# Optimization experiments

Hardware: AMD Instinct MI355X
Metric: run time of the kernel (lower is better)

Reference implementation:

```python
import jax, jax.numpy as jnp
import numpy as np
import math

B, LQ, LK = 2, 2048, 2048
DIM = 1024
H = 16
DH = DIM // H


def setup_inputs() -> dict:
    key = jax.random.key(0)
    ks = jax.random.split(key, 12)
    s = 1.0 / math.sqrt(DIM)
    return {
        "query": jax.random.normal(ks[0], (B, LQ, DIM), jnp.float32),
        "key": jax.random.normal(ks[1], (B, LK, DIM), jnp.float32),
        "value": jax.random.normal(ks[2], (B, LK, DIM), jnp.float32),
        "mask": jnp.zeros((B, LQ, LK), dtype=bool),
        "Wq": jax.random.normal(ks[3], (DIM, DIM), jnp.float32) * s,
        "bq": jax.random.normal(ks[4], (DIM,), jnp.float32) * s,
        "Wk": jax.random.normal(ks[5], (DIM, DIM), jnp.float32) * s,
        "bk": jax.random.normal(ks[6], (DIM,), jnp.float32) * s,
        "Wv": jax.random.normal(ks[7], (DIM, DIM), jnp.float32) * s,
        "bv": jax.random.normal(ks[8], (DIM,), jnp.float32) * s,
        "Wo": jax.random.normal(ks[9], (DIM, DIM), jnp.float32) * s,
        "bo": jax.random.normal(ks[10], (DIM,), jnp.float32) * s,
    }


def reference(query, key, value, mask, Wq, bq, Wk, bk, Wv, bv, Wo, bo):
    b = query.shape[0]

    def shape(x):  # (b, l, dim) -> (b, h, l, dh)
        return x.reshape(b, -1, H, DH).transpose(0, 2, 1, 3)

    q = shape(query @ Wq.T + bq)
    k = shape(key @ Wk.T + bk)
    v = shape(value @ Wv.T + bv)

    q = q / math.sqrt(DH)
    # (b, h, lq, lk) score matrix, computed in float32 as the original does
    scores = jnp.einsum("bhqd,bhkd->bhqk", q, k).astype(jnp.float32)
    scores = jnp.where(mask[:, None, :, :], jnp.float32(-1e18), scores)
    attn = jax.nn.softmax(scores, axis=-1).astype(q.dtype)
    context = jnp.einsum("bhqk,bhkd->bhqd", attn, v)
    context = context.transpose(0, 2, 1, 3).reshape(b, -1, H * DH)
    return context @ Wo.T + bo
```

## Files before the change

kernel.cpp:

```cpp
#include <hip/hip_runtime.h>
#include <hip/hip_bf16.h>

typedef __attribute__((ext_vector_type(4))) float float4v;
typedef __attribute__((ext_vector_type(8))) __bf16 bf16x8;
typedef __attribute__((ext_vector_type(4))) unsigned short ushort4v;

#define MFMA16(a, b, c) __builtin_amdgcn_mfma_f32_16x16x32_bf16(a, b, c, 0, 0, 0)

__device__ __forceinline__ unsigned short f2bf(float f) {
    return __builtin_bit_cast(unsigned short, (__bf16)f);
}

__device__ __forceinline__ float fast_exp2(float x) {
#if __has_builtin(__builtin_amdgcn_exp2f)
    return __builtin_amdgcn_exp2f(x);
#else
    return exp2f(x);
#endif
}

__device__ __forceinline__ void gl_lds16(const unsigned short* g, unsigned short* l) {
    __builtin_amdgcn_global_load_lds(
        (const __attribute__((address_space(1))) void*)g,
        (__attribute__((address_space(3))) void*)l, 16, 0, 0);
}

__device__ __forceinline__ uint4 pack8bf(float4v a0, float4v a1) {
    uint4 u;
    u.x = (unsigned int)f2bf(a0.x) | ((unsigned int)f2bf(a0.y) << 16);
    u.y = (unsigned int)f2bf(a0.z) | ((unsigned int)f2bf(a0.w) << 16);
    u.z = (unsigned int)f2bf(a1.x) | ((unsigned int)f2bf(a1.y) << 16);
    u.w = (unsigned int)f2bf(a1.z) | ((unsigned int)f2bf(a1.w) << 16);
    return u;
}

struct CvtSeg { const float* s; unsigned short* d; int n; };
struct Cvt4 { CvtSeg seg[4]; };

__global__ __launch_bounds__(256) void cvt_kernel(Cvt4 a) {
    const CvtSeg c = a.seg[blockIdx.y];
    const int stride = gridDim.x * 256 * 4;
    for (int i = (blockIdx.x * 256 + threadIdx.x) * 4; i < c.n; i += stride) {
        float4v v = *(const float4v*)(c.s + i);
        ushort4v u;
        u.x = f2bf(v.x); u.y = f2bf(v.y); u.z = f2bf(v.z); u.w = f2bf(v.w);
        *(ushort4v*)(c.d + i) = u;
    }
}

__global__ __launch_bounds__(256) void gemm_qkv_kernel(
    const float* qa, const float* ka, const float* va,
    const unsigned short* Wqb, const unsigned short* Wkb, const unsigned short* Wvb,
    const float* bq, const float* bk, const float* bv,
    unsigned short* Qb, unsigned short* Kb, unsigned short* Vtg, float qscale) {
    __shared__ unsigned short Sm[17408];
    unsigned short* As = Sm;
    unsigned short* Ws = Sm + 8192;

    const int z = blockIdx.z;
    const float* A = z == 0 ? qa : (z == 1 ? ka : va);
    const unsigned short* W = z == 0 ? Wqb : (z == 1 ? Wkb : Wvb);
    const float* bias = z == 0 ? bq : (z == 1 ? bk : bv);
    const float scale = z == 0 ? qscale : 1.0f;

    const int K = 1024, N = 1024;
    const int t = threadIdx.x;
    const int w = t >> 6, lane = t & 63;
    const int quad = lane >> 4, l16 = lane & 15;
    const int m0 = blockIdx.x * 128, n0 = blockIdx.y * 128;
    const int wm = (w >> 1) * 64, wn = (w & 1) * 64;

    float4v acc[4][4];
    for (int i = 0; i < 4; ++i)
        for (int j = 0; j < 4; ++j) acc[i][j] = float4v{0.f, 0.f, 0.f, 0.f};

    const int arow = t >> 3, acol = (t & 7) * 8;
    const int srow = lane >> 3, scol = (lane & 7) * 8;

    for (int k0 = 0; k0 < K; k0 += 64) {
        __syncthreads();
        for (int p = 0; p < 4; ++p) {
            const int r = arow + p * 32;
            const float* ap = A + (size_t)(m0 + r) * K + k0 + acol;
            float4v a0 = *(const float4v*)ap;
            float4v a1 = *(const float4v*)(ap + 4);
            *(uint4*)&As[r * 64 + acol] = pack8bf(a0, a1);
        }
        for (int i = 0; i < 4; ++i) {
            const int c = w * 4 + i;
            gl_lds16(W + (size_t)(n0 + c * 8 + srow) * K + k0 + scol,
                     &Ws[c * 512 + lane * 8]);
        }
        __syncthreads();
        for (int ks = 0; ks < 2; ++ks) {
            bf16x8 af[4], wf[4];
            for (int i = 0; i < 4; ++i)
                af[i] = *(const bf16x8*)&As[(wm + i * 16 + l16) * 64 + ks * 32 + quad * 8];
            for (int i = 0; i < 4; ++i)
                wf[i] = *(const bf16x8*)&Ws[(wn + i * 16 + l16) * 64 + ks * 32 + quad * 8];
            for (int mi = 0; mi < 4; ++mi)
                for (int ni = 0; ni < 4; ++ni)
                    acc[mi][ni] = MFMA16(af[mi], wf[ni], acc[mi][ni]);
        }
    }

    if (z < 2) {
        unsigned short* C = z == 0 ? Qb : Kb;
        for (int mi = 0; mi < 4; ++mi)
            for (int ni = 0; ni < 4; ++ni) {
                const int col = n0 + wn + ni * 16 + l16;
                const float bvv = bias[col];
                for (int reg = 0; reg < 4; ++reg) {
                    const int row = m0 + wm + mi * 16 + quad * 4 + reg;
                    C[(size_t)row * N + col] = f2bf((acc[mi][ni][reg] + bvv) * scale);
                }
            }
    } else {
        __syncthreads();
        for (int mi = 0; mi < 4; ++mi)
            for (int ni = 0; ni < 4; ++ni) {
                const int col = wn + ni * 16 + l16;
                const float bvv = bias[n0 + col];
                for (int reg = 0; reg < 4; ++reg) {
                    const int row = wm + mi * 16 + quad * 4 + reg;
                    Sm[col * 136 + row] = f2bf(acc[mi][ni][reg] + bvv);
                }
            }
        __syncthreads();
        const int col = t >> 1, rb = (t & 1) * 64;
        for (int j = 0; j < 8; ++j) {
            uint4 v = *(const uint4*)&Sm[col * 136 + rb + j * 8];
            *(uint4*)&Vtg[(size_t)(n0 + col) * 4096 + m0 + rb + j * 8] = v;
        }
    }
}

__global__ __launch_bounds__(256) void gemm_out_kernel(const unsigned short* __restrict__ A,
                                                       const unsigned short* __restrict__ W,
                                                       const float* __restrict__ bias,
                                                       float* __restrict__ Cout) {
    __shared__ unsigned short As[64 * 64];
    __shared__ unsigned short Ws[128 * 64];
    const int N = 1024, K = 1024;
    const int t = threadIdx.x;
    const int w = t >> 6, lane = t & 63;
    const int quad = lane >> 4, l16 = lane & 15;
    const int m0 = blockIdx.x * 64, n0 = blockIdx.y * 128;
    const int wm = (w & 1) * 32, wn = (w >> 1) * 64;

    float4v acc[2][4];
    for (int i = 0; i < 2; ++i)
        for (int j = 0; j < 4; ++j) acc[i][j] = float4v{0.f, 0.f, 0.f, 0.f};

    const int srow = lane >> 3;
    const int scol = (lane & 7) * 8;

    for (int k0 = 0; k0 < K; k0 += 64) {
        __syncthreads();
        for (int i = 0; i < 2; ++i) {
            const int c = w * 2 + i;
            gl_lds16(A + (size_t)(m0 + c * 8 + srow) * K + k0 + scol,
                     &As[c * 512 + lane * 8]);
        }
        for (int i = 0; i < 4; ++i) {
            const int c = w * 4 + i;
            gl_lds16(W + (size_t)(n0 + c * 8 + srow) * K + k0 + scol,
                     &Ws[c * 512 + lane * 8]);
        }
        __syncthreads();
        for (int ks = 0; ks < 2; ++ks) {
            bf16x8 af[2], wf[4];
            for (int i = 0; i < 2; ++i)
                af[i] = *(const bf16x8*)&As[(wm + i * 16 + l16) * 64 + ks * 32 + quad * 8];
            for (int i = 0; i < 4; ++i)
                wf[i] = *(const bf16x8*)&Ws[(wn + i * 16 + l16) * 64 + ks * 32 + quad * 8];
            for (int mi = 0; mi < 2; ++mi)
                for (int ni = 0; ni < 4; ++ni)
                    acc[mi][ni] = MFMA16(af[mi], wf[ni], acc[mi][ni]);
        }
    }

    for (int mi = 0; mi < 2; ++mi)
        for (int ni = 0; ni < 4; ++ni) {
            const int col = n0 + wn + ni * 16 + l16;
            const float bv = bias[col];
            for (int reg = 0; reg < 4; ++reg) {
                const int row = m0 + wm + mi * 16 + quad * 4 + reg;
                Cout[(size_t)row * N + col] = acc[mi][ni][reg] + bv;
            }
        }
}

__global__ __launch_bounds__(256) void attn_kernel(const unsigned short* __restrict__ Q,
                                                   const unsigned short* __restrict__ Kg,
                                                   const unsigned short* __restrict__ Vtg,
                                                   const unsigned char* __restrict__ mask,
                                                   unsigned short* __restrict__ Ctx) {
    const int bid = blockIdx.x;
    const int bh = bid & 31;
    const int qt = bid >> 5;
    const int b = bh >> 4, h = bh & 15;
    const int t = threadIdx.x, w = t >> 6, lane = t & 63;
    const int quad = lane >> 4, l16 = lane & 15;

    __shared__ unsigned short Pt[128][72];
    __shared__ unsigned short Ks[64][72];
    __shared__ unsigned short Vt[64][72];

    const unsigned short* Qp = Q + ((size_t)(b * 2048 + qt * 128)) * 1024 + h * 64;
    const unsigned short* Kp = Kg + ((size_t)b * 2048) * 1024 + h * 64;
    const unsigned short* Vp = Vtg + (size_t)(h * 64) * 4096 + b * 2048;
    const unsigned char* Mp = mask + (size_t)(b * 2048 + qt * 128) * 2048;

    for (int p = 0; p < 4; ++p) {
        const int idx = t + p * 256;
        const int r = idx >> 3, c8 = (idx & 7) * 8;
        *(uint4*)&Pt[r][c8] = *(const uint4*)(Qp + (size_t)r * 1024 + c8);
    }
    __syncthreads();
    bf16x8 qf[2][2];
    for (int c = 0; c < 2; ++c)
        for (int ks = 0; ks < 2; ++ks)
            qf[c][ks] = *(const bf16x8*)&Pt[w * 32 + c * 16 + l16][ks * 32 + quad * 8];

    float4v o[2][4];
    for (int c = 0; c < 2; ++c)
        for (int i = 0; i < 4; ++i) o[c][i] = float4v{0.f, 0.f, 0.f, 0.f};
    float l_acc[2] = {0.f, 0.f};

    const int sr = t >> 3, sc8 = (t & 7) * 8;
    const int vd = t >> 2, vs0 = (t & 3) * 16;
    const int mrow = w * 32 + (lane >> 1);
    const int mc0 = (lane & 1) * 32;

    uint4 kreg0, kreg1, vreg0, vreg1, mreg0, mreg1;
    {
        kreg0 = *(const uint4*)(Kp + (size_t)sr * 1024 + sc8);
        kreg1 = *(const uint4*)(Kp + (size_t)(sr + 32) * 1024 + sc8);
        vreg0 = *(const uint4*)(Vp + (size_t)vd * 4096 + vs0);
        vreg1 = *(const uint4*)(Vp + (size_t)vd * 4096 + vs0 + 8);
        mreg0 = *(const uint4*)(Mp + (size_t)mrow * 2048 + mc0);
        mreg1 = *(const uint4*)(Mp + (size_t)mrow * 2048 + mc0 + 16);
    }

    for (int kc = 0; kc < 2048; kc += 64) {
        __syncthreads();
        *(uint4*)&Ks[sr][sc8] = kreg0;
        *(uint4*)&Ks[sr + 32][sc8] = kreg1;
        *(uint4*)&Vt[vd][vs0] = vreg0;
        *(uint4*)&Vt[vd][vs0 + 8] = vreg1;
        const unsigned int mor = mreg0.x | mreg0.y | mreg0.z | mreg0.w |
                                 mreg1.x | mreg1.y | mreg1.z | mreg1.w;
        const bool anymask = __any(mor != 0);
        __syncthreads();

        const int kn = kc + 64;
        if (kn < 2048) {
            kreg0 = *(const uint4*)(Kp + (size_t)(kn + sr) * 1024 + sc8);
            kreg1 = *(const uint4*)(Kp + (size_t)(kn + sr + 32) * 1024 + sc8);
            vreg0 = *(const uint4*)(Vp + (size_t)vd * 4096 + kn + vs0);
            vreg1 = *(const uint4*)(Vp + (size_t)vd * 4096 + kn + vs0 + 8);
            mreg0 = *(const uint4*)(Mp + (size_t)mrow * 2048 + kn + mc0);
            mreg1 = *(const uint4*)(Mp + (size_t)mrow * 2048 + kn + mc0 + 16);
        }

        float4v s0[4], s1[4];
        for (int nt = 0; nt < 4; ++nt) {
            const float4v z4 = float4v{0.f, 0.f, 0.f, 0.f};
            bf16x8 kf = *(const bf16x8*)&Ks[nt * 16 + l16][quad * 8];
            s0[nt] = MFMA16(kf, qf[0][0], z4);
            s1[nt] = MFMA16(kf, qf[1][0], z4);
            kf = *(const bf16x8*)&Ks[nt * 16 + l16][32 + quad * 8];
            s0[nt] = MFMA16(kf, qf[0][1], s0[nt]);
            s1[nt] = MFMA16(kf, qf[1][1], s1[nt]);
        }

        for (int c = 0; c < 2; ++c) {
            float4v* s = c ? s1 : s0;
            const int qrow = w * 32 + c * 16 + l16;
            float lc = l_acc[c];
            for (int nt = 0; nt < 4; ++nt) {
                float p0 = s[nt][0], p1 = s[nt][1], p2 = s[nt][2], p3 = s[nt][3];
                if (anymask) {
                    const unsigned char* mr =
                        Mp + (size_t)qrow * 2048 + kc + nt * 16 + quad * 4;
                    if (mr[0]) p0 = -1e18f;
                    if (mr[1]) p1 = -1e18f;
                    if (mr[2]) p2 = -1e18f;
                    if (mr[3]) p3 = -1e18f;
                }
                const float e0 = fast_exp2(p0), e1 = fast_exp2(p1);
                const float e2 = fast_exp2(p2), e3 = fast_exp2(p3);
                lc += (e0 + e1) + (e2 + e3);
                uint2 u;
                u.x = (unsigned int)f2bf(e0) | ((unsigned int)f2bf(e1) << 16);
                u.y = (unsigned int)f2bf(e2) | ((unsigned int)f2bf(e3) << 16);
                *(uint2*)&Pt[qrow][nt * 16 + quad * 4] = u;
            }
            l_acc[c] = lc;
        }

        for (int ks = 0; ks < 2; ++ks) {
            bf16x8 pf0 = *(const bf16x8*)&Pt[w * 32 + l16][ks * 32 + quad * 8];
            bf16x8 pf1 = *(const bf16x8*)&Pt[w * 32 + 16 + l16][ks * 32 + quad * 8];
            for (int dt = 0; dt < 4; ++dt) {
                bf16x8 vf = *(const bf16x8*)&Vt[dt * 16 + l16][ks * 32 + quad * 8];
                o[0][dt] = MFMA16(pf0, vf, o[0][dt]);
                o[1][dt] = MFMA16(pf1, vf, o[1][dt]);
            }
        }
    }

    float lfull[2];
    for (int c = 0; c < 2; ++c) {
        float l = l_acc[c];
        l += __shfl_xor(l, 16);
        l += __shfl_xor(l, 32);
        lfull[c] = l;
    }

    for (int c = 0; c < 2; ++c) {
        float inv[4];
        for (int reg = 0; reg < 4; ++reg)
            inv[reg] = 1.0f / __shfl(lfull[c], (lane & 48) | (quad * 4 + reg));
        for (int dt = 0; dt < 4; ++dt) {
            const int dcol = dt * 16 + l16;
            for (int reg = 0; reg < 4; ++reg) {
                const int ql = w * 32 + c * 16 + quad * 4 + reg;
                Ctx[((size_t)(b * 2048 + qt * 128 + ql)) * 1024 + h * 64 + dcol] =
                    f2bf(o[c][dt][reg] * inv[reg]);
            }
        }
    }
}

extern "C" void kernel_launch(void* const* d_in, const int* in_sizes, int n_in,
                              void* d_out, int out_size, void* d_ws, size_t ws_size,
                              hipStream_t stream) {
    (void)in_sizes; (void)n_in; (void)out_size; (void)ws_size;
    const float* query = (const float*)d_in[0];
    const float* key   = (const float*)d_in[1];
    const float* value = (const float*)d_in[2];
    const unsigned char* mask = (const unsigned char*)d_in[3];
    const float* Wq = (const float*)d_in[4];
    const float* bq = (const float*)d_in[5];
    const float* Wk = (const float*)d_in[6];
    const float* bk = (const float*)d_in[7];
    const float* Wv = (const float*)d_in[8];
    const float* bv = (const float*)d_in[9];
    const float* Wo = (const float*)d_in[10];
    const float* bo = (const float*)d_in[11];

    const size_t MD = (size_t)4096 * 1024;
    const size_t WD = (size_t)1024 * 1024;

    unsigned short* Qb  = (unsigned short*)d_ws;
    unsigned short* Kb  = Qb + MD;
    unsigned short* Vtg = Kb + MD;
    unsigned short* Wqb = Vtg + MD;
    unsigned short* Wkb = Wqb + WD;
    unsigned short* Wvb = Wkb + WD;
    unsigned short* Wob = Wvb + WD;
    unsigned short* Cb  = Wob + WD;

    Cvt4 cv;
    cv.seg[0] = {Wq, Wqb, (int)WD};
    cv.seg[1] = {Wk, Wkb, (int)WD};
    cv.seg[2] = {Wv, Wvb, (int)WD};
    cv.seg[3] = {Wo, Wob, (int)WD};
    cvt_kernel<<<dim3(256, 4), 256, 0, stream>>>(cv);

    const float qscale = 0.125f * 1.44269504088896f;
    gemm_qkv_kernel<<<dim3(32, 8, 3), 256, 0, stream>>>(
        query, key, value, Wqb, Wkb, Wvb, bq, bk, bv, Qb, Kb, Vtg, qscale);

    attn_kernel<<<dim3(512), 256, 0, stream>>>(Qb, Kb, Vtg, mask, Cb);

    gemm_out_kernel<<<dim3(64, 8), 256, 0, stream>>>(Cb, Wob, bo, (float*)d_out);
}
```

Measured before the change: 287.0 us.

## Register-prefetch next K tile in projection GEMMs instead of direct global-to-LDS loads

Both the QKV projection GEMM and the output projection GEMM stop using global_load_lds for each K tile. They now load the next tile's A and W slices into registers while the MFMA loop runs on the current tile, then write them to LDS at the start of the next iteration. This is meant to hide global memory latency behind compute. The cost is extra registers for the prefetch buffers, which may lower occupancy, and extra LDS store instructions.

```diff
diff --git a/kernel.cpp b/kernel.cpp
--- a/kernel.cpp
+++ b/kernel.cpp
@@ -17,12 +17,6 @@
 #else
     return exp2f(x);
 #endif
-}
-
-__device__ __forceinline__ void gl_lds16(const unsigned short* g, unsigned short* l) {
-    __builtin_amdgcn_global_load_lds(
-        (const __attribute__((address_space(1))) void*)g,
-        (__attribute__((address_space(3))) void*)l, 16, 0, 0);
 }
 
 __device__ __forceinline__ uint4 pack8bf(float4v a0, float4v a1) {
@@ -77,21 +71,41 @@
     const int arow = t >> 3, acol = (t & 7) * 8;
     const int srow = lane >> 3, scol = (lane & 7) * 8;
 
-    for (int k0 = 0; k0 < K; k0 += 64) {
-        __syncthreads();
+    float4v apre[4][2];
+    uint4 wpre[4];
+    {
         for (int p = 0; p < 4; ++p) {
-            const int r = arow + p * 32;
-            const float* ap = A + (size_t)(m0 + r) * K + k0 + acol;
-            float4v a0 = *(const float4v*)ap;
-            float4v a1 = *(const float4v*)(ap + 4);
-            *(uint4*)&As[r * 64 + acol] = pack8bf(a0, a1);
+            const float* ap = A + (size_t)(m0 + arow + p * 32) * K + acol;
+            apre[p][0] = *(const float4v*)ap;
+            apre[p][1] = *(const float4v*)(ap + 4);
         }
         for (int i = 0; i < 4; ++i) {
             const int c = w * 4 + i;
-            gl_lds16(W + (size_t)(n0 + c * 8 + srow) * K + k0 + scol,
-                     &Ws[c * 512 + lane * 8]);
-        }
-        __syncthreads();
+            wpre[i] = *(const uint4*)(W + (size_t)(n0 + c * 8 + srow) * K + scol);
+        }
+    }
+
+    for (int k0 = 0; k0 < K; k0 += 64) {
+        __syncthreads();
+        for (int p = 0; p < 4; ++p)
+            *(uint4*)&As[(arow + p * 32) * 64 + acol] = pack8bf(apre[p][0], apre[p][1]);
+        for (int i = 0; i < 4; ++i)
+            *(uint4*)&Ws[(w * 4 + i) * 512 + lane * 8] = wpre[i];
+        __syncthreads();
+
+        const int kn = k0 + 64;
+        if (kn < K) {
+            for (int p = 0; p < 4; ++p) {
+                const float* ap = A + (size_t)(m0 + arow + p * 32) * K + kn + acol;
+                apre[p][0] = *(const float4v*)ap;
+                apre[p][1] = *(const float4v*)(ap + 4);
+            }
+            for (int i = 0; i < 4; ++i) {
+                const int c = w * 4 + i;
+                wpre[i] = *(const uint4*)(W + (size_t)(n0 + c * 8 + srow) * K + kn + scol);
+            }
+        }
+
         for (int ks = 0; ks < 2; ++ks) {
             bf16x8 af[4], wf[4];
             for (int i = 0; i < 4; ++i)
@@ -155,19 +169,38 @@
     const int srow = lane >> 3;
     const int scol = (lane & 7) * 8;
 
-    for (int k0 = 0; k0 < K; k0 += 64) {
-        __syncthreads();
+    uint4 apre[2], wpre[4];
+    {
         for (int i = 0; i < 2; ++i) {
             const int c = w * 2 + i;
-            gl_lds16(A + (size_t)(m0 + c * 8 + srow) * K + k0 + scol,
-                     &As[c * 512 + lane * 8]);
+            apre[i] = *(const uint4*)(A + (size_t)(m0 + c * 8 + srow) * K + scol);
         }
         for (int i = 0; i < 4; ++i) {
             const int c = w * 4 + i;
-            gl_lds16(W + (size_t)(n0 + c * 8 + srow) * K + k0 + scol,
-                     &Ws[c * 512 + lane * 8]);
-        }
-        __syncthreads();
+            wpre[i] = *(const uint4*)(W + (size_t)(n0 + c * 8 + srow) * K + scol);
+        }
+    }
+
+    for (int k0 = 0; k0 < K; k0 += 64) {
+        __syncthreads();
+        for (int i = 0; i < 2; ++i)
+            *(uint4*)&As[(w * 2 + i) * 512 + lane * 8] = apre[i];
+        for (int i = 0; i < 4; ++i)
+            *(uint4*)&Ws[(w * 4 + i) * 512 + lane * 8] = wpre[i];
+        __syncthreads();
+
+        const int kn = k0 + 64;
+        if (kn < K) {
+            for (int i = 0; i < 2; ++i) {
+                const int c = w * 2 + i;
+                apre[i] = *(const uint4*)(A + (size_t)(m0 + c * 8 + srow) * K + kn + scol);
+            }
+            for (int i = 0; i < 4; ++i) {
+                const int c = w * 4 + i;
+                wpre[i] = *(const uint4*)(W + (size_t)(n0 + c * 8 + srow) * K + kn + scol);
+            }
+        }
+
         for (int ks = 0; ks < 2; ++ks) {
             bf16x8 af[2], wf[4];
             for (int i = 0; i < 2; ++i)
```

Result: slower. 344.3 us (+19.9%).
